# Kernel optimization log

Hardware: AMD Instinct MI355X
Metric: run time of the kernel (lower is better)

The kernel has to match this reference:

```python
import jax, jax.numpy as jnp
import numpy as np

D_MODEL = 4096
D_FF = 11008
M = 8192
GROUP = 128
NLEVELS = 16  # 4-bit


def setup_inputs() -> dict:
    key = jax.random.key(0)
    ks = jax.random.split(key, 10)
    def qw(k, K, N):
        return jax.random.randint(k, (K, N), 0, NLEVELS, dtype=jnp.int32)
    def qz(k, G, N):
        return jax.random.randint(k, (G, N), 0, NLEVELS, dtype=jnp.int32)
    def sc(k, G, N):
        # small positive per-group scales, roughly matching real AWQ magnitudes
        return jax.random.uniform(k, (G, N), dtype=jnp.float32) * 0.02 + 1e-3
    return {
        "x": jax.random.normal(ks[0], (M, D_MODEL), dtype=jnp.float32),
        "q_gate": qw(ks[1], D_MODEL, D_FF),
        "z_gate": qz(ks[2], D_MODEL // GROUP, D_FF),
        "s_gate": sc(ks[3], D_MODEL // GROUP, D_FF),
        "q_up": qw(ks[4], D_MODEL, D_FF),
        "z_up": qz(ks[5], D_MODEL // GROUP, D_FF),
        "s_up": sc(ks[6], D_MODEL // GROUP, D_FF),
        "q_down": qw(ks[7], D_FF, D_MODEL),
        "z_down": qz(ks[8], D_FF // GROUP, D_MODEL),
        "s_down": sc(ks[9], D_FF // GROUP, D_MODEL),
        "group_size": GROUP,
    }


def _dequant(q, z, s, group_size):
    # q: [K, N] int4 values; z: [K//G, N] zeros; s: [K//G, N] scales
    K, N = q.shape
    G = group_size
    w = (q.astype(s.dtype).reshape(K // G, G, N) - z.astype(s.dtype)[:, None, :]) * s[:, None, :]
    return w.reshape(K, N)


def reference(x, q_gate, z_gate, s_gate, q_up, z_up, s_up, q_down, z_down, s_down, group_size):
    gate = x @ _dequant(q_gate, z_gate, s_gate, group_size)   # [M, D_FF]
    up = x @ _dequant(q_up, z_up, s_up, group_size)           # [M, D_FF]
    h = jax.nn.silu(gate) * up                                # SwiGLU
    return h @ _dequant(q_down, z_down, s_down, group_size)   # [M, D_MODEL]
```

## Files before the change

kernel.cpp:

```cpp
#include <hip/hip_runtime.h>
#include <cstdint>

typedef unsigned short u16;
typedef unsigned int u32;
typedef unsigned char u8;
typedef signed char s8;
typedef __bf16 bf16_t;
typedef bf16_t bf16x8 __attribute__((ext_vector_type(8)));
typedef float f32x4 __attribute__((ext_vector_type(4)));
typedef int i32x4 __attribute__((ext_vector_type(4)));

#define DMODEL 4096
#define DFF 11008
#define MROWS 8192

__device__ __forceinline__ u16 f2bf(float f) {
  u32 u = __builtin_bit_cast(u32, f);
  u += 0x7FFFu + ((u >> 16) & 1u);
  return (u16)(u >> 16);
}
__device__ __forceinline__ float bf2f(u16 h) {
  return __builtin_bit_cast(float, (u32)h << 16);
}

#define GLD16(gptr, lptr)                                                  \
  __builtin_amdgcn_global_load_lds(                                        \
      (const __attribute__((address_space(1))) u32*)(gptr),                \
      (__attribute__((address_space(3))) u32*)(lptr), 16, 0, 0)

#define BAR asm volatile("s_barrier" ::: "memory")
#define VM0 asm volatile("s_waitcnt vmcnt(0)" ::: "memory")
#define VM4 asm volatile("s_waitcnt vmcnt(4)" ::: "memory")
#define LGKM0 asm volatile("s_waitcnt lgkmcnt(0)" ::: "memory")

__global__ void k_quant_x(const float* __restrict__ x, s8* __restrict__ x8,
                          float* __restrict__ sx) {
  const int row = blockIdx.x;
  const int t = threadIdx.x;
  const int lane = t & 63, wid = t >> 6;
  const float4* xr = reinterpret_cast<const float4*>(x + (size_t)row * DMODEL);
  float4 v[4];
  float m = 0.f;
#pragma unroll
  for (int i = 0; i < 4; ++i) {
    v[i] = xr[t * 4 + i];
    m = fmaxf(m, fmaxf(fmaxf(fabsf(v[i].x), fabsf(v[i].y)),
                       fmaxf(fabsf(v[i].z), fabsf(v[i].w))));
  }
#pragma unroll
  for (int off = 32; off >= 1; off >>= 1) m = fmaxf(m, __shfl_xor(m, off));
  __shared__ float wm[4];
  if (lane == 0) wm[wid] = m;
  __syncthreads();
  float mall = fmaxf(fmaxf(wm[0], wm[1]), fmaxf(wm[2], wm[3]));
  mall = fmaxf(mall, 1e-8f);
  const float inv = 127.f / mall;
  if (t == 0) sx[row] = mall / 127.f;
  uint4 o;
  u32 p[4];
#pragma unroll
  for (int i = 0; i < 4; ++i) {
    int a = (int)rintf(v[i].x * inv), b = (int)rintf(v[i].y * inv);
    int c = (int)rintf(v[i].z * inv), d = (int)rintf(v[i].w * inv);
    p[i] = (u32)(a & 255) | ((u32)(b & 255) << 8) | ((u32)(c & 255) << 16) |
           ((u32)(d & 255) << 24);
  }
  o.x = p[0]; o.y = p[1]; o.z = p[2]; o.w = p[3];
  reinterpret_cast<uint4*>(x8 + (size_t)row * DMODEL)[t] = o;
}

__global__ void k_dequant_T8(const int* __restrict__ q, const int* __restrict__ z,
                             s8* __restrict__ w8, int K, int N) {
  __shared__ s8 tile[32][40];
  const int t = threadIdx.x;
  const int n0 = blockIdx.x << 5, k0 = blockIdx.y << 5;
  {
    const int kr = t >> 3, n4 = (t & 7) << 2;
    const int k = k0 + kr, g = k >> 7;
    const int4 qv = *reinterpret_cast<const int4*>(&q[(size_t)k * N + n0 + n4]);
    const int4 zv = *reinterpret_cast<const int4*>(&z[(size_t)g * N + n0 + n4]);
    tile[kr][n4 + 0] = (s8)(qv.x - zv.x);
    tile[kr][n4 + 1] = (s8)(qv.y - zv.y);
    tile[kr][n4 + 2] = (s8)(qv.z - zv.z);
    tile[kr][n4 + 3] = (s8)(qv.w - zv.w);
  }
  __syncthreads();
  {
    const int n = t >> 3, ks = (t & 7) << 2;
    uchar4 o;
    o.x = (u8)tile[ks + 0][n];
    o.y = (u8)tile[ks + 1][n];
    o.z = (u8)tile[ks + 2][n];
    o.w = (u8)tile[ks + 3][n];
    *reinterpret_cast<uchar4*>(&w8[(size_t)(n0 + n) * K + k0 + ks]) = o;
  }
}

__global__ void k_dequant_T(const int* __restrict__ q, const int* __restrict__ z,
                            const float* __restrict__ s, u16* __restrict__ wT,
                            int K, int N) {
  __shared__ u16 tile[32][36];
  const int t = threadIdx.x;
  const int n0 = blockIdx.x << 5, k0 = blockIdx.y << 5;
  {
    const int kr = t >> 3, n4 = (t & 7) << 2;
    const int k = k0 + kr, g = k >> 7;
    const int4 qv = *reinterpret_cast<const int4*>(&q[(size_t)k * N + n0 + n4]);
    const int4 zv = *reinterpret_cast<const int4*>(&z[(size_t)g * N + n0 + n4]);
    const float4 sv = *reinterpret_cast<const float4*>(&s[(size_t)g * N + n0 + n4]);
    ushort4 o;
    o.x = f2bf((float)(qv.x - zv.x) * sv.x);
    o.y = f2bf((float)(qv.y - zv.y) * sv.y);
    o.z = f2bf((float)(qv.z - zv.z) * sv.z);
    o.w = f2bf((float)(qv.w - zv.w) * sv.w);
    *reinterpret_cast<ushort4*>(&tile[kr][n4]) = o;
  }
  __syncthreads();
  {
    const int n = t >> 3, ks = (t & 7) << 2;
    ushort4 o;
    o.x = tile[ks + 0][n];
    o.y = tile[ks + 1][n];
    o.z = tile[ks + 2][n];
    o.w = tile[ks + 3][n];
    *reinterpret_cast<ushort4*>(&wT[(size_t)(n0 + n) * K + k0 + ks]) = o;
  }
}

__global__ __launch_bounds__(512, 2) void k_fused_i8(
    const s8* __restrict__ A, const s8* __restrict__ Bg,
    const s8* __restrict__ Bu, const float* __restrict__ sx,
    const float* __restrict__ sg, const float* __restrict__ su,
    u16* __restrict__ H) {
  constexpr int Kdim = DMODEL;
  constexpr int ntiles = Kdim >> 6;
  __shared__ s8 Ab[2][2][256 * 64];
  __shared__ s8 Bgb[2][2][128 * 64];
  __shared__ s8 Bub[2][2][128 * 64];
  __shared__ u16 sclh[2][32 * 128];

  const int midx = blockIdx.x & 31, nidx = blockIdx.x >> 5;
  const int m0 = midx << 8, n0 = nidx << 7;
  const int t = threadIdx.x;
  const int lane = t & 63;
  const int wid = t >> 6;
  const int wr = wid >> 2, wc = wid & 3;
  const int r16 = lane & 15, quad = lane >> 4;

  const int lrow = lane >> 2;
  const int sswz = ((lane & 3) ^ ((lrow >> 1) & 3)) << 4;
  const s8* Asrc = A + (size_t)(m0 + wid * 16 + lrow) * Kdim + sswz;
  const s8* Gsrc = Bg + (size_t)(n0 + wid * 16 + lrow) * Kdim + sswz;
  const s8* Usrc = Bu + (size_t)(n0 + wid * 16 + lrow) * Kdim + sswz;
  const size_t rstepA = (size_t)128 * Kdim;
  const int ldst = wid * 1024;

#define STG(tt, pb_, ti) do {                                              \
    size_t ko = (size_t)((tt) & (ntiles - 1)) << 6;                        \
    GLD16(Asrc + ko,          &Ab[pb_][ti][ldst]);                         \
    GLD16(Asrc + ko + rstepA, &Ab[pb_][ti][ldst + 8192]);                  \
    GLD16(Gsrc + ko,          &Bgb[pb_][ti][ldst]);                        \
    GLD16(Usrc + ko,          &Bub[pb_][ti][ldst]);                        \
  } while (0)

  const int aswz = (quad ^ ((r16 >> 1) & 3)) << 4;
  const int abase = (wr * 128 + r16) * 64 + aswz;
  const int bbase = (wc * 32 + r16) * 64 + aswz;

  f32x4 facg[8][2], facu[8][2];
  const f32x4 zf = {0.f, 0.f, 0.f, 0.f};
#pragma unroll
  for (int mf = 0; mf < 8; ++mf)
#pragma unroll
    for (int nf = 0; nf < 2; ++nf) { facg[mf][nf] = zf; facu[mf][nf] = zf; }
  const i32x4 zi = {0, 0, 0, 0};

#pragma unroll
  for (int k = 0; k < 2; ++k) {
    int j = t + k * 512;
    int g = j >> 5;
    int c = (j & 31) << 2;
    float4 vg = *reinterpret_cast<const float4*>(&sg[(size_t)g * DFF + n0 + c]);
    float4 vu = *reinterpret_cast<const float4*>(&su[(size_t)g * DFF + n0 + c]);
    ushort4 og, ou;
    og.x = f2bf(vg.x); og.y = f2bf(vg.y); og.z = f2bf(vg.z); og.w = f2bf(vg.w);
    ou.x = f2bf(vu.x); ou.y = f2bf(vu.y); ou.z = f2bf(vu.z); ou.w = f2bf(vu.w);
    *reinterpret_cast<ushort4*>(&sclh[0][g * 128 + c]) = og;
    *reinterpret_cast<ushort4*>(&sclh[1][g * 128 + c]) = ou;
  }
  STG(0, 0, 0); STG(1, 0, 1);
  VM0;
  LGKM0;
  BAR;

  const int sloc = wc * 32 + r16;

  for (int i = 0; i < (ntiles >> 1); ++i) {
    const int pb = i & 1;
    i32x4 av0[8], bg_a[2], bg_b[2], bu_a[2], bu_b[2];
#pragma unroll
    for (int mf = 0; mf < 8; ++mf)
      av0[mf] = *reinterpret_cast<const i32x4*>(&Ab[pb][0][abase + mf * 1024]);
#pragma unroll
    for (int nf = 0; nf < 2; ++nf) {
      bg_a[nf] = *reinterpret_cast<const i32x4*>(&Bgb[pb][0][bbase + nf * 1024]);
      bu_a[nf] = *reinterpret_cast<const i32x4*>(&Bub[pb][0][bbase + nf * 1024]);
      bg_b[nf] = *reinterpret_cast<const i32x4*>(&Bgb[pb][1][bbase + nf * 1024]);
      bu_b[nf] = *reinterpret_cast<const i32x4*>(&Bub[pb][1][bbase + nf * 1024]);
    }
    float s_g0 = bf2f(sclh[0][i * 128 + sloc]);
    float s_g1 = bf2f(sclh[0][i * 128 + sloc + 16]);
    float s_u0 = bf2f(sclh[1][i * 128 + sloc]);
    float s_u1 = bf2f(sclh[1][i * 128 + sloc + 16]);
    STG(2 * i + 2, pb ^ 1, 0);
    STG(2 * i + 3, pb ^ 1, 1);
    __builtin_amdgcn_s_setprio(1);
#pragma unroll
    for (int mf = 0; mf < 8; ++mf) {
      i32x4 a1 = *reinterpret_cast<const i32x4*>(&Ab[pb][1][abase + mf * 1024]);
      i32x4 ig0 = __builtin_amdgcn_mfma_i32_16x16x64_i8(av0[mf], bg_a[0], zi, 0, 0, 0);
      i32x4 ig1 = __builtin_amdgcn_mfma_i32_16x16x64_i8(av0[mf], bg_a[1], zi, 0, 0, 0);
      i32x4 iu0 = __builtin_amdgcn_mfma_i32_16x16x64_i8(av0[mf], bu_a[0], zi, 0, 0, 0);
      i32x4 iu1 = __builtin_amdgcn_mfma_i32_16x16x64_i8(av0[mf], bu_a[1], zi, 0, 0, 0);
      ig0 = __builtin_amdgcn_mfma_i32_16x16x64_i8(a1, bg_b[0], ig0, 0, 0, 0);
      ig1 = __builtin_amdgcn_mfma_i32_16x16x64_i8(a1, bg_b[1], ig1, 0, 0, 0);
      iu0 = __builtin_amdgcn_mfma_i32_16x16x64_i8(a1, bu_b[0], iu0, 0, 0, 0);
      iu1 = __builtin_amdgcn_mfma_i32_16x16x64_i8(a1, bu_b[1], iu1, 0, 0, 0);
#pragma unroll
      for (int j = 0; j < 4; ++j) {
        facg[mf][0][j] += (float)ig0[j] * s_g0;
        facg[mf][1][j] += (float)ig1[j] * s_g1;
        facu[mf][0][j] += (float)iu0[j] * s_u0;
        facu[mf][1][j] += (float)iu1[j] * s_u1;
      }
    }
    __builtin_amdgcn_s_setprio(0);
    VM0;
    BAR;
  }

  const int rb0 = m0 + wr * 128 + quad * 4;
  const int cb0 = n0 + wc * 32 + r16;
#pragma unroll
  for (int mf = 0; mf < 8; ++mf) {
#pragma unroll
    for (int j = 0; j < 4; ++j) {
      const int row = rb0 + mf * 16 + j;
      const float sxr = sx[row];
#pragma unroll
      for (int nf = 0; nf < 2; ++nf) {
        float gv = facg[mf][nf][j] * sxr;
        float uv = facu[mf][nf][j] * sxr;
        float sv = gv / (1.f + __expf(-gv));
        H[(size_t)row * DFF + cb0 + nf * 16] = f2bf(sv * uv);
      }
    }
  }
#undef STG
}

__global__ __launch_bounds__(512, 2) void k_down(
    const u16* __restrict__ A, const u16* __restrict__ BT,
    float* __restrict__ C) {
  constexpr int Ndim = DMODEL, Kdim = DFF;
  __shared__ u16 As[2][2][256 * 32];
  __shared__ u16 Bs[2][2][256 * 32];

  const int nidx = blockIdx.x & 15;
  const int midx = blockIdx.x >> 4;
  const int m0 = midx << 8;
  const int n0 = nidx << 8;
  const int t = threadIdx.x;
  const int lane = t & 63;
  const int wid = t >> 6;
  const int wr = wid >> 2, wc = wid & 3;
  const int r16 = lane & 15, quad = lane >> 4;

  const int lrow4 = lane >> 2;
  const int sslot = ((lane & 3) ^ ((lane >> 3) & 3)) << 3;
  const u16* Asrc = A + (size_t)(m0 + wid * 16 + lrow4) * Kdim + sslot;
  const u16* Bsrc = BT + (size_t)(n0 + wid * 16 + lrow4) * Kdim + sslot;
  const size_t rstep = (size_t)128 * Kdim;
  const int lbo = wid * 512;
  constexpr int ntiles = Kdim >> 6;

#define SA(tt, kh, bf) do {                                                \
    int ttw = (tt) < ntiles ? (tt) : (tt) - ntiles;                        \
    size_t ko = ((size_t)ttw << 6) + ((kh) << 5);                          \
    GLD16(Asrc + ko,         &As[bf][kh][lbo]);                            \
    GLD16(Asrc + ko + rstep, &As[bf][kh][lbo + 4096]);                     \
  } while (0)
#define SB(tt, kh, bf) do {                                                \
    int ttw = (tt) < ntiles ? (tt) : (tt) - ntiles;                        \
    size_t ko = ((size_t)ttw << 6) + ((kh) << 5);                          \
    GLD16(Bsrc + ko,         &Bs[bf][kh][lbo]);                            \
    GLD16(Bsrc + ko + rstep, &Bs[bf][kh][lbo + 4096]);                     \
  } while (0)

  const int fragoff = (quad ^ ((r16 >> 1) & 3)) << 3;
  const int abase = (wr * 128 + r16) * 32 + fragoff;
  const int bbase = (wc * 64 + r16) * 32 + fragoff;

  f32x4 acc[8][4];
  const f32x4 zf = {0.f, 0.f, 0.f, 0.f};
#pragma unroll
  for (int mf = 0; mf < 8; ++mf)
#pragma unroll
    for (int nf = 0; nf < 4; ++nf) acc[mf][nf] = zf;

  bf16x8 avA[4], av2A[4], bvA[4];
  bf16x8 avB[4], av2B[4], bvB[4];

#define PFD(av_, av2_, bv_, bf, kk) do {                                   \
    _Pragma("unroll") for (int ii = 0; ii < 4; ++ii) {                     \
      av_[ii] = *reinterpret_cast<const bf16x8*>(                          \
          &As[bf][kk][abase + ii * 512]);                                  \
      av2_[ii] = *reinterpret_cast<const bf16x8*>(                         \
          &As[bf][kk][abase + 2048 + ii * 512]);                           \
    }                                                                      \
    _Pragma("unroll") for (int nn = 0; nn < 4; ++nn)                       \
      bv_[nn] = *reinterpret_cast<const bf16x8*>(                          \
          &Bs[bf][kk][bbase + nn * 512]);                                  \
  } while (0)

#define PHD(av_, av2_, bv_, nav_, nav2_, nbv_, STG_, VMW, bfn, kkn) do {   \
    STG_;                                                                  \
    VMW;                                                                   \
    BAR;                                                                   \
    __builtin_amdgcn_s_setprio(1);                                         \
    _Pragma("unroll") for (int ii = 0; ii < 4; ++ii)                       \
      _Pragma("unroll") for (int nn = 0; nn < 4; ++nn)                     \
        acc[ii][nn] = __builtin_amdgcn_mfma_f32_16x16x32_bf16(             \
            av_[ii], bv_[nn], acc[ii][nn], 0, 0, 0);                       \
    PFD(nav_, nav2_, nbv_, bfn, kkn);                                      \
    _Pragma("unroll") for (int ii = 0; ii < 4; ++ii)                       \
      _Pragma("unroll") for (int nn = 0; nn < 4; ++nn)                     \
        acc[4 + ii][nn] = __builtin_amdgcn_mfma_f32_16x16x32_bf16(         \
            av2_[ii], bv_[nn], acc[4 + ii][nn], 0, 0, 0);                  \
    __builtin_amdgcn_s_setprio(0);                                         \
    BAR;                                                                   \
  } while (0)

  SA(0, 0, 0); SB(0, 0, 0); SA(0, 1, 0); SB(0, 1, 0); SA(1, 0, 1); SB(1, 0, 1);
  VM4;
  BAR;
  PFD(avA, av2A, bvA, 0, 0);

  constexpr int NI = ntiles >> 1;
  for (int it = 0; it < NI; ++it) {
    const int t0 = it * 2;
    PHD(avA, av2A, bvA, avB, av2B, bvB,
        { SA(t0 + 1, 1, 1); SB(t0 + 1, 1, 1); }, (void)0, 0, 1);
    PHD(avB, av2B, bvB, avA, av2A, bvA,
        { SA(t0 + 2, 0, 0); SB(t0 + 2, 0, 0); }, VM4, 1, 0);
    PHD(avA, av2A, bvA, avB, av2B, bvB,
        { SA(t0 + 2, 1, 0); SB(t0 + 2, 1, 0); }, (void)0, 1, 1);
    PHD(avB, av2B, bvB, avA, av2A, bvA,
        { SA(t0 + 3, 0, 1); SB(t0 + 3, 0, 1); }, VM4, 0, 0);
  }
  asm volatile("s_waitcnt vmcnt(0)" ::: "memory");

  const int rb0 = m0 + wr * 128 + quad * 4;
  const int cb0 = n0 + wc * 64 + r16;
#pragma unroll
  for (int mf = 0; mf < 8; ++mf) {
#pragma unroll
    for (int nf = 0; nf < 4; ++nf) {
      f32x4 v = acc[mf][nf];
      int row = rb0 + mf * 16;
      int col = cb0 + nf * 16;
#pragma unroll
      for (int j = 0; j < 4; ++j)
        C[(size_t)(row + j) * Ndim + col] = v[j];
    }
  }
#undef SA
#undef SB
#undef PFD
#undef PHD
}

extern "C" void kernel_launch(void* const* d_in, const int* in_sizes, int n_in,
                              void* d_out, int out_size, void* d_ws, size_t ws_size,
                              hipStream_t stream) {
  const float* x  = (const float*)d_in[0];
  const int*   qg = (const int*)d_in[1];
  const int*   zg = (const int*)d_in[2];
  const float* sg = (const float*)d_in[3];
  const int*   qu = (const int*)d_in[4];
  const int*   zu = (const int*)d_in[5];
  const float* su = (const float*)d_in[6];
  const int*   qd = (const int*)d_in[7];
  const int*   zd = (const int*)d_in[8];
  const float* sd = (const float*)d_in[9];
  float* out = (float*)d_out;

  char* ws = (char*)d_ws;
  const size_t szX8 = (size_t)MROWS * DMODEL;
  const size_t szSX = (size_t)MROWS * 4;
  const size_t szW8 = (size_t)DMODEL * DFF;
  const size_t szWD = (size_t)DFF * DMODEL * 2;
  s8*    x8  = (s8*)(ws);
  float* sx  = (float*)(ws + szX8);
  s8*    wg8 = (s8*)(ws + szX8 + szSX);
  s8*    wu8 = (s8*)(ws + szX8 + szSX + szW8);
  u16*   wdT = (u16*)(ws + szX8 + szSX + 2 * szW8);
  u16*   h   = (u16*)(ws + szX8 + szSX + 2 * szW8 + szWD);

  k_quant_x<<<MROWS, 256, 0, stream>>>(x, x8, sx);
  k_dequant_T8<<<dim3(DFF / 32, DMODEL / 32), 256, 0, stream>>>(qg, zg, wg8, DMODEL, DFF);
  k_dequant_T8<<<dim3(DFF / 32, DMODEL / 32), 256, 0, stream>>>(qu, zu, wu8, DMODEL, DFF);
  k_dequant_T<<<dim3(DMODEL / 32, DFF / 32), 256, 0, stream>>>(qd, zd, sd, wdT, DFF, DMODEL);

  k_fused_i8<<<(MROWS / 256) * (DFF / 128), 512, 0, stream>>>(
      x8, wg8, wu8, sx, sg, su, h);
  k_down<<<(MROWS / 256) * (DMODEL / 256), 512, 0, stream>>>(h, wdT, out);
}
```

Before: 1.824 ms.

## Replace half-tile ping-pong pipeline with simple full-tile double-buffer loop

```diff
diff --git a/kernel.cpp b/kernel.cpp
--- a/kernel.cpp
+++ b/kernel.cpp
@@ -30,7 +30,6 @@
 
 #define BAR asm volatile("s_barrier" ::: "memory")
 #define VM0 asm volatile("s_waitcnt vmcnt(0)" ::: "memory")
-#define VM4 asm volatile("s_waitcnt vmcnt(4)" ::: "memory")
 #define LGKM0 asm volatile("s_waitcnt lgkmcnt(0)" ::: "memory")
 
 __global__ void k_quant_x(const float* __restrict__ x, s8* __restrict__ x8,
@@ -308,57 +307,44 @@
 #pragma unroll
     for (int nf = 0; nf < 4; ++nf) acc[mf][nf] = zf;
 
-  bf16x8 avA[4], av2A[4], bvA[4];
-  bf16x8 avB[4], av2B[4], bvB[4];
-
-#define PFD(av_, av2_, bv_, bf, kk) do {                                   \
-    _Pragma("unroll") for (int ii = 0; ii < 4; ++ii) {                     \
-      av_[ii] = *reinterpret_cast<const bf16x8*>(                          \
-          &As[bf][kk][abase + ii * 512]);                                  \
-      av2_[ii] = *reinterpret_cast<const bf16x8*>(                         \
-          &As[bf][kk][abase + 2048 + ii * 512]);                           \
-    }                                                                      \
-    _Pragma("unroll") for (int nn = 0; nn < 4; ++nn)                       \
-      bv_[nn] = *reinterpret_cast<const bf16x8*>(                          \
-          &Bs[bf][kk][bbase + nn * 512]);                                  \
-  } while (0)
-
-#define PHD(av_, av2_, bv_, nav_, nav2_, nbv_, STG_, VMW, bfn, kkn) do {   \
-    STG_;                                                                  \
-    VMW;                                                                   \
-    BAR;                                                                   \
-    __builtin_amdgcn_s_setprio(1);                                         \
-    _Pragma("unroll") for (int ii = 0; ii < 4; ++ii)                       \
-      _Pragma("unroll") for (int nn = 0; nn < 4; ++nn)                     \
-        acc[ii][nn] = __builtin_amdgcn_mfma_f32_16x16x32_bf16(             \
-            av_[ii], bv_[nn], acc[ii][nn], 0, 0, 0);                       \
-    PFD(nav_, nav2_, nbv_, bfn, kkn);                                      \
-    _Pragma("unroll") for (int ii = 0; ii < 4; ++ii)                       \
-      _Pragma("unroll") for (int nn = 0; nn < 4; ++nn)                     \
-        acc[4 + ii][nn] = __builtin_amdgcn_mfma_f32_16x16x32_bf16(         \
-            av2_[ii], bv_[nn], acc[4 + ii][nn], 0, 0, 0);                  \
-    __builtin_amdgcn_s_setprio(0);                                         \
-    BAR;                                                                   \
-  } while (0)
-
-  SA(0, 0, 0); SB(0, 0, 0); SA(0, 1, 0); SB(0, 1, 0); SA(1, 0, 1); SB(1, 0, 1);
-  VM4;
+  SA(0, 0, 0); SB(0, 0, 0); SA(0, 1, 0); SB(0, 1, 0);
+  VM0;
   BAR;
-  PFD(avA, av2A, bvA, 0, 0);
-
-  constexpr int NI = ntiles >> 1;
-  for (int it = 0; it < NI; ++it) {
-    const int t0 = it * 2;
-    PHD(avA, av2A, bvA, avB, av2B, bvB,
-        { SA(t0 + 1, 1, 1); SB(t0 + 1, 1, 1); }, (void)0, 0, 1);
-    PHD(avB, av2B, bvB, avA, av2A, bvA,
-        { SA(t0 + 2, 0, 0); SB(t0 + 2, 0, 0); }, VM4, 1, 0);
-    PHD(avA, av2A, bvA, avB, av2B, bvB,
-        { SA(t0 + 2, 1, 0); SB(t0 + 2, 1, 0); }, (void)0, 1, 1);
-    PHD(avB, av2B, bvB, avA, av2A, bvA,
-        { SA(t0 + 3, 0, 1); SB(t0 + 3, 0, 1); }, VM4, 0, 0);
-  }
-  asm volatile("s_waitcnt vmcnt(0)" ::: "memory");
+
+  for (int tt = 0; tt < ntiles; ++tt) {
+    const int bf = tt & 1;
+    bf16x8 a0[8], b0[4], b1[4];
+#pragma unroll
+    for (int mf = 0; mf < 8; ++mf)
+      a0[mf] = *reinterpret_cast<const bf16x8*>(&As[bf][0][abase + mf * 512]);
+#pragma unroll
+    for (int nf = 0; nf < 4; ++nf) {
+      b0[nf] = *reinterpret_cast<const bf16x8*>(&Bs[bf][0][bbase + nf * 512]);
+      b1[nf] = *reinterpret_cast<const bf16x8*>(&Bs[bf][1][bbase + nf * 512]);
+    }
+    SA(tt + 1, 0, bf ^ 1); SB(tt + 1, 0, bf ^ 1);
+    SA(tt + 1, 1, bf ^ 1); SB(tt + 1, 1, bf ^ 1);
+    __builtin_amdgcn_s_setprio(1);
+#pragma unroll
+    for (int mf = 0; mf < 8; ++mf)
+#pragma unroll
+      for (int nf = 0; nf < 4; ++nf)
+        acc[mf][nf] = __builtin_amdgcn_mfma_f32_16x16x32_bf16(
+            a0[mf], b0[nf], acc[mf][nf], 0, 0, 0);
+    bf16x8 a1[8];
+#pragma unroll
+    for (int mf = 0; mf < 8; ++mf)
+      a1[mf] = *reinterpret_cast<const bf16x8*>(&As[bf][1][abase + mf * 512]);
+#pragma unroll
+    for (int mf = 0; mf < 8; ++mf)
+#pragma unroll
+      for (int nf = 0; nf < 4; ++nf)
+        acc[mf][nf] = __builtin_amdgcn_mfma_f32_16x16x32_bf16(
+            a1[mf], b1[nf], acc[mf][nf], 0, 0, 0);
+    __builtin_amdgcn_s_setprio(0);
+    VM0;
+    BAR;
+  }
 
   const int rb0 = m0 + wr * 128 + quad * 4;
   const int cb0 = n0 + wc * 64 + r16;
@@ -376,8 +362,6 @@
   }
 #undef SA
 #undef SB
-#undef PFD
-#undef PHD
 }
 
 extern "C" void kernel_launch(void* const* d_in, const int* in_sizes, int n_in,
```

Result: faster. 1.753 ms (median of 2 runs) (-3.9%).
